# Optimization experiments

Measured on AMD Instinct MI355X. Metric: run time of the kernel, lower is better.

Reference implementation:

```python
import jax, jax.numpy as jnp
import numpy as np

B, I, C, L, KS = 16, 64, 128, 16384, 5
CA_K = 5
K_CR = 76      # crucial channels: floor(0.6*128)=76, already even
EPS = 1e-5


def conv1d(x, w, pad):
    # x: [N, Cin, L], w: [Cout, Cin, K]
    return jax.lax.conv_general_dilated(
        x, w, window_strides=(1,), padding=[(pad, pad)],
        dimension_numbers=('NCH', 'OIH', 'NCH'))


def bn(x, g, b, m, v):
    # eval-mode BatchNorm1d over channel dim of [N, C, L]
    inv = g / jnp.sqrt(v + EPS)
    return x * inv[None, :, None] + (b - m * inv)[None, :, None]


def setup_inputs() -> dict:
    key = jax.random.key(0)
    ks = jax.random.split(key, 10)
    return {
        'x': jax.random.normal(ks[0], (B, I, L), jnp.float32),
        'conv_w': jax.random.normal(ks[1], (C, I, KS), jnp.float32) / np.sqrt(I * KS).astype(np.float32),
        'conv_b': jax.random.normal(ks[2], (C,), jnp.float32) * 0.01,
        'bn_g': jnp.ones((C,), jnp.float32) + jax.random.normal(ks[3], (C,), jnp.float32) * 0.05,
        'bn_b': jax.random.normal(ks[4], (C,), jnp.float32) * 0.05,
        'bn_m': jax.random.normal(ks[5], (C,), jnp.float32) * 0.05,
        'bn_v': jnp.ones((C,), jnp.float32) + jax.random.uniform(ks[6], (C,), jnp.float32) * 0.1,
        'alpha': jnp.float32(0.5),
        'beta': jnp.float32(0.5),
        'ca_w': jax.random.normal(ks[7], (1, 1, CA_K), jnp.float32) / np.sqrt(CA_K).astype(np.float32),
        'ca_b': jnp.zeros((1,), jnp.float32),
        'sa_w': jax.random.normal(ks[8], (1, 2, 7), jnp.float32) / np.sqrt(14.0).astype(np.float32),
        'sabn_g': jnp.ones((1,), jnp.float32) + jax.random.normal(ks[9], (1,), jnp.float32) * 0.05,
        'sabn_b': jnp.zeros((1,), jnp.float32),
        'sabn_m': jnp.zeros((1,), jnp.float32),
        'sabn_v': jnp.ones((1,), jnp.float32),
    }


def reference(x, conv_w, conv_b, bn_g, bn_b, bn_m, bn_v, alpha, beta,
              ca_w, ca_b, sa_w, sabn_g, sabn_b, sabn_m, sabn_v):
    # ---- conv_layer: Conv1d + BN + ReLU ----
    f = conv1d(x, conv_w, KS // 2) + conv_b[None, :, None]      # [B,C,L]
    f = jax.nn.relu(bn(f, bn_g, bn_b, bn_m, bn_v))

    # ---- ChannelAttention ----
    F_avg = jnp.mean(f, axis=2, keepdims=True)                  # [B,C,1]
    F_max = jnp.max(f, axis=2, keepdims=True)                   # [B,C,1]
    F_add = alpha * F_avg + 0.5 * (F_avg + F_max) + beta * F_max
    z = conv1d(F_add.transpose(0, 2, 1), ca_w, CA_K // 2) + ca_b[None, :, None]  # [B,1,C]
    channel_map = jax.nn.sigmoid(z.transpose(0, 2, 1))          # [B,C,1]

    crf = f * channel_map                                       # channel refined features

    # ---- SpatialAttention: topk channel split + scatter masks ----
    cm = channel_map[:, :, 0]                                   # [B,C]
    _, idx = jax.lax.top_k(cm, K_CR)                            # [B,K_CR]
    cru = jnp.zeros_like(cm).at[jnp.arange(B)[:, None], idx].set(1.0)[:, :, None]  # [B,C,1]
    sub = 1.0 - cru

    cf = cru * crf                                              # crucial features [B,C,L]
    sf = sub * crf                                              # subcrucial features

    c_max = jnp.max(cf, axis=1, keepdims=True)                  # [B,1,L]
    c_avg = jnp.mean(cf, axis=1, keepdims=True) * (C / K_CR)
    s_max = jnp.max(sf, axis=1, keepdims=True)
    s_avg = jnp.mean(sf, axis=1, keepdims=True) * (C / (C - K_CR))

    def gate(mx, av):
        y = conv1d(jnp.concatenate([mx, av], axis=1), sa_w, 3)  # [B,1,L]
        return jax.nn.sigmoid(jax.nn.relu(bn(y, sabn_g, sabn_b, sabn_m, sabn_v)))

    A1 = gate(c_max, c_avg)
    A2 = gate(s_max, s_avg)
    return cf * A1 + sf * A2                                    # [B,C,L]
```

## Files before the change

kernel.cpp:

```cpp
#include <hip/hip_runtime.h>
#include <hip/hip_bf16.h>
#include <math.h>

#define BB 16
#define IC 64
#define CH 128
#define LL 16384
#define KS 5
#define CAK 5
#define KCR 76
#define EPSV 1e-5f
#define NLT2 256

typedef short bf16x8 __attribute__((ext_vector_type(8)));
typedef float f32x16 __attribute__((ext_vector_type(16)));

#define OFF_WPACK 0
#define OFF_BIAS2 40960
#define OFF_PSUM  (OFF_BIAS2 + CH)
#define OFF_PMAX  (OFF_PSUM + BB*CH*NLT2)
#define OFF_CM    (OFF_PMAX + BB*CH*NLT2)
#define OFF_MASK  (OFF_CM + BB*CH)
#define OFF_A1    (OFF_MASK + BB*CH)
#define OFF_A2    (OFF_A1 + BB*LL)
#define OFF_F16   (OFF_A2 + BB*LL)
#define WS_NEED_FLOATS ((size_t)OFF_F16 + (size_t)BB * CH * LL / 2)

__device__ __forceinline__ unsigned short f2bf(float f) {
    union { float f; unsigned u; } v; v.f = f;
    return (unsigned short)((v.u + 0x7FFFu + ((v.u >> 16) & 1u)) >> 16);
}
__device__ __forceinline__ float bf2f(unsigned short h) {
    union { unsigned u; float f; } v; v.u = ((unsigned)h) << 16;
    return v.f;
}
__device__ __forceinline__ unsigned short f2h(float f) {
    _Float16 h = (_Float16)f;
    return __builtin_bit_cast(unsigned short, h);
}
__device__ __forceinline__ float h2f(unsigned short u) {
    _Float16 h = __builtin_bit_cast(_Float16, u);
    return (float)h;
}

template<int CTRL>
__device__ __forceinline__ float dppf(float v) {
    return __builtin_bit_cast(float,
        __builtin_amdgcn_update_dpp(0, __builtin_bit_cast(int, v), CTRL, 0xF, 0xF, true));
}
__device__ __forceinline__ float dpp_sum32(float s) {
    s += dppf<0x111>(s);
    s += dppf<0x112>(s);
    s += dppf<0x114>(s);
    s += dppf<0x118>(s);
    s += dppf<0x142>(s);
    return s;
}
__device__ __forceinline__ float dpp_max32(float m) {
    m = fmaxf(m, dppf<0x111>(m));
    m = fmaxf(m, dppf<0x112>(m));
    m = fmaxf(m, dppf<0x114>(m));
    m = fmaxf(m, dppf<0x118>(m));
    m = fmaxf(m, dppf<0x142>(m));
    return m;
}

__global__ void prep_kernel(const float* __restrict__ conv_w, const float* __restrict__ conv_b,
                            const float* __restrict__ bn_g, const float* __restrict__ bn_b,
                            const float* __restrict__ bn_m, const float* __restrict__ bn_v,
                            unsigned short* __restrict__ wpack, float* __restrict__ bias2)
{
    int e = blockIdx.x * 256 + threadIdx.x;
    if (e < 8 * 20 * 64 * 8) {
        int j    = e & 7;
        int ln   = (e >> 3) & 63;
        int rest = e >> 9;
        int s    = rest % 20;
        int mt   = (rest / 20) & 1;
        int ch2  = (rest / 40) & 1;
        int ver  = rest / 80;
        int c  = ch2 * 64 + mt * 32 + (ln & 31);
        int kk = s >> 2;
        int i  = (s & 3) * 16 + (ln >> 5) * 8 + j;
        float inv = bn_g[c] * rsqrtf(bn_v[c] + EPSV);
        float w = conv_w[(c * IC + i) * KS + kk] * inv;
        unsigned short h = f2bf(w);
        wpack[e] = (ver == 0) ? h : f2bf(w - bf2f(h));
    }
    if (e < CH) {
        float inv = bn_g[e] * rsqrtf(bn_v[e] + EPSV);
        bias2[e] = (conv_b[e] - bn_m[e]) * inv + bn_b[e];
    }
}

template<bool F16OUT>
__global__ __launch_bounds__(256, 4)
void conv_mfma_kernel(const float* __restrict__ x,
                      const unsigned short* __restrict__ wpack,
                      const float* __restrict__ bias2,
                      void* __restrict__ fout,
                      float* __restrict__ psum, float* __restrict__ pmax)
{
    __shared__ unsigned short xs[136 * 128];
    const int b   = blockIdx.x;
    const int lt  = blockIdx.y;
    const int l0  = lt * 128;
    const int tid = threadIdx.x;
    const int ln  = tid & 63;
    const int wv  = __builtin_amdgcn_readfirstlane(tid >> 6);

    const float* xb = x + (size_t)b * (IC * LL);
    const int ibase = wv * 16;
    #pragma unroll
    for (int g = 0; g < 3; ++g) {
        int row = g * 64 + ln;
        int l   = l0 - 4 + row;
        if (row < 136) {
            bool vl = (l >= 0) && (l < LL);
            float v[16];
            #pragma unroll
            for (int q = 0; q < 16; ++q)
                v[q] = vl ? xb[(size_t)(ibase + q) * LL + l] : 0.0f;
            int rs = row & 7;
            #pragma unroll
            for (int q2 = 0; q2 < 4; ++q2) {
                unsigned short h[4], lo[4];
                #pragma unroll
                for (int j = 0; j < 4; ++j) {
                    float vv = v[q2 * 4 + j];
                    h[j]  = f2bf(vv);
                    lo[j] = f2bf(vv - bf2f(h[j]));
                }
                int i0   = ibase + q2 * 4;
                int cc   = (i0 >> 3) ^ rs;
                int epos = row * 128 + cc * 8 + (i0 & 7);
                uint2 wh, wl;
                wh.x = (unsigned)h[0]  | ((unsigned)h[1]  << 16);
                wh.y = (unsigned)h[2]  | ((unsigned)h[3]  << 16);
                wl.x = (unsigned)lo[0] | ((unsigned)lo[1] << 16);
                wl.y = (unsigned)lo[2] | ((unsigned)lo[3] << 16);
                *(uint2*)&xs[epos]      = wh;
                *(uint2*)&xs[epos + 64] = wl;
            }
        }
    }
    __syncthreads();

    const int ch2  = wv >> 1;
    const int lh   = wv & 1;
    const int ln31 = ln & 31;
    const int hi   = ln >> 5;
    const int rowbase = lh * 64 + ln31 + 2;

    const unsigned short* wp  = wpack + (size_t)ln * 8;
    const unsigned short* pA0 = wp + (size_t)((ch2 * 2 + 0) * 20) * 512;
    const unsigned short* pA1 = wp + (size_t)((ch2 * 2 + 1) * 20) * 512;
    const unsigned short* pA2 = wp + (size_t)(((2 + ch2) * 2 + 0) * 20) * 512;
    const unsigned short* pA3 = wp + (size_t)(((2 + ch2) * 2 + 1) * 20) * 512;

    f32x16 acc[2][2];
    #pragma unroll
    for (int mt = 0; mt < 2; ++mt)
        #pragma unroll
        for (int nt = 0; nt < 2; ++nt)
            #pragma unroll
            for (int r = 0; r < 16; ++r) acc[mt][nt][r] = 0.0f;

    auto loadA = [&](bf16x8* Av, int s) {
        Av[0] = *(const bf16x8*)(pA0 + (size_t)s * 512);
        Av[1] = *(const bf16x8*)(pA1 + (size_t)s * 512);
        Av[2] = *(const bf16x8*)(pA2 + (size_t)s * 512);
        Av[3] = *(const bf16x8*)(pA3 + (size_t)s * 512);
    };
    auto loadB = [&](bf16x8* Bv, int s) {
        int kk = s >> 2, iq = s & 3;
        int r0 = rowbase + kk;
        int r1 = r0 + 32;
        int c0 = ((iq << 1) + hi) ^ (r0 & 7);
        int c1 = ((iq << 1) + hi) ^ (r1 & 7);
        Bv[0] = *(const bf16x8*)&xs[r0 * 128 + c0 * 8];
        Bv[1] = *(const bf16x8*)&xs[r0 * 128 + 64 + c0 * 8];
        Bv[2] = *(const bf16x8*)&xs[r1 * 128 + c1 * 8];
        Bv[3] = *(const bf16x8*)&xs[r1 * 128 + 64 + c1 * 8];
    };
    auto compute = [&](const bf16x8* Av, const bf16x8* Bv) {
        acc[0][0] = __builtin_amdgcn_mfma_f32_32x32x16_bf16(Av[0], Bv[0], acc[0][0], 0, 0, 0);
        acc[1][0] = __builtin_amdgcn_mfma_f32_32x32x16_bf16(Av[1], Bv[0], acc[1][0], 0, 0, 0);
        acc[0][1] = __builtin_amdgcn_mfma_f32_32x32x16_bf16(Av[0], Bv[2], acc[0][1], 0, 0, 0);
        acc[1][1] = __builtin_amdgcn_mfma_f32_32x32x16_bf16(Av[1], Bv[2], acc[1][1], 0, 0, 0);
        acc[0][0] = __builtin_amdgcn_mfma_f32_32x32x16_bf16(Av[0], Bv[1], acc[0][0], 0, 0, 0);
        acc[1][0] = __builtin_amdgcn_mfma_f32_32x32x16_bf16(Av[1], Bv[1], acc[1][0], 0, 0, 0);
        acc[0][1] = __builtin_amdgcn_mfma_f32_32x32x16_bf16(Av[0], Bv[3], acc[0][1], 0, 0, 0);
        acc[1][1] = __builtin_amdgcn_mfma_f32_32x32x16_bf16(Av[1], Bv[3], acc[1][1], 0, 0, 0);
        acc[0][0] = __builtin_amdgcn_mfma_f32_32x32x16_bf16(Av[2], Bv[0], acc[0][0], 0, 0, 0);
        acc[1][0] = __builtin_amdgcn_mfma_f32_32x32x16_bf16(Av[3], Bv[0], acc[1][0], 0, 0, 0);
        acc[0][1] = __builtin_amdgcn_mfma_f32_32x32x16_bf16(Av[2], Bv[2], acc[0][1], 0, 0, 0);
        acc[1][1] = __builtin_amdgcn_mfma_f32_32x32x16_bf16(Av[3], Bv[2], acc[1][1], 0, 0, 0);
    };

    bf16x8 Ar[3][4], Br[2][4];
    loadA(Ar[0], 0); loadA(Ar[1], 1); loadA(Ar[2], 2);
    loadB(Br[0], 0); loadB(Br[1], 1);
    #pragma unroll
    for (int s = 0; s < 20; ++s) {
        compute(Ar[s % 3], Br[s & 1]);
        if (s + 3 < 20) loadA(Ar[s % 3], s + 3);
        if (s + 2 < 20) loadB(Br[s & 1], s + 2);
    }

    const int lgbase = l0 + lh * 64 + ln31;
    #pragma unroll
    for (int mt = 0; mt < 2; ++mt) {
        #pragma unroll
        for (int nt = 0; nt < 2; ++nt) {
            #pragma unroll
            for (int r = 0; r < 16; ++r) {
                int c = ch2 * 64 + mt * 32 + (r & 3) + 8 * (r >> 2) + 4 * hi;
                float fv = fmaxf(acc[mt][nt][r] + bias2[c], 0.0f);
                size_t off = ((size_t)(b * CH + c)) * LL + lgbase + nt * 32;
                if constexpr (F16OUT) ((unsigned short*)fout)[off] = f2h(fv);
                else                  ((float*)fout)[off] = fv;
                acc[mt][nt][r] = fv;
            }
        }
    }
    #pragma unroll
    for (int mt = 0; mt < 2; ++mt) {
        #pragma unroll
        for (int r = 0; r < 16; ++r) {
            float s = dpp_sum32(acc[mt][0][r] + acc[mt][1][r]);
            float m = dpp_max32(fmaxf(acc[mt][0][r], acc[mt][1][r]));
            if (ln31 == 31) {
                int c   = ch2 * 64 + mt * 32 + (r & 3) + 8 * (r >> 2) + 4 * hi;
                int lt2 = lt * 2 + lh;
                psum[(b * CH + c) * NLT2 + lt2] = s;
                pmax[(b * CH + c) * NLT2 + lt2] = m;
            }
        }
    }
}

__global__ void chan_kernel(const float* __restrict__ psum, const float* __restrict__ pmax,
                            const float* __restrict__ alpha, const float* __restrict__ beta,
                            const float* __restrict__ ca_w, const float* __restrict__ ca_b,
                            float* __restrict__ cm, float* __restrict__ maskv)
{
    int b = blockIdx.x;
    int c = threadIdx.x;
    const float* ps = psum + (b * CH + c) * NLT2;
    const float* pm = pmax + (b * CH + c) * NLT2;
    float s = 0.0f, m = 0.0f;
    for (int t = 0; t < NLT2; ++t) { s += ps[t]; m = fmaxf(m, pm[t]); }
    float favg = s * (1.0f / LL);
    float fadd = (alpha[0] + 0.5f) * favg + (beta[0] + 0.5f) * m;

    __shared__ float fa[CH];
    __shared__ float cms[CH];
    fa[c] = fadd;
    __syncthreads();

    float z = ca_b[0];
    #pragma unroll
    for (int k = 0; k < CAK; ++k) {
        int cc = c + k - 2;
        float v = (cc >= 0 && cc < CH) ? fa[cc] : 0.0f;
        z = fmaf(ca_w[k], v, z);
    }
    float cmv = 1.0f / (1.0f + expf(-z));
    cms[c] = cmv;
    __syncthreads();

    int rank = 0;
    for (int cc = 0; cc < CH; ++cc) {
        float o = cms[cc];
        rank += (o > cmv || (o == cmv && cc < c)) ? 1 : 0;
    }
    cm[b * CH + c] = cmv;
    maskv[b * CH + c] = (rank < KCR) ? 1.0f : 0.0f;
}

__global__ __launch_bounds__(256)
void sgf_kernel(const unsigned short* __restrict__ f16, float* __restrict__ out,
                const float* __restrict__ cm, const float* __restrict__ maskv,
                const float* __restrict__ sa_w,
                const float* __restrict__ sabn_g, const float* __restrict__ sabn_b,
                const float* __restrict__ sabn_m, const float* __restrict__ sabn_v)
{
    __shared__ float cms[CH], mks[CH];
    __shared__ float st[4][520];
    const int g   = blockIdx.x;
    const int b   = blockIdx.y;
    const int l0  = g * 512;
    const int tid = threadIdx.x;
    if (tid < CH) { cms[tid] = cm[b * CH + tid]; mks[tid] = maskv[b * CH + tid]; }
    __syncthreads();

    {
        const unsigned short* fb = f16 + (size_t)b * CH * LL + l0 + 2 * tid;
        float cmx0 = 0.f, csm0 = 0.f, smx0 = 0.f, ssm0 = 0.f;
        float cmx1 = 0.f, csm1 = 0.f, smx1 = 0.f, ssm1 = 0.f;
        #pragma unroll 4
        for (int c = 0; c < CH; ++c) {
            unsigned pr = *(const unsigned*)(fb + (size_t)c * LL);
            float cmc = cms[c], mk = mks[c];
            float v0 = h2f((unsigned short)(pr & 0xFFFFu)) * cmc;
            float v1 = h2f((unsigned short)(pr >> 16)) * cmc;
            float vs0 = v0 * mk, vu0 = v0 - vs0;
            float vs1 = v1 * mk, vu1 = v1 - vs1;
            cmx0 = fmaxf(cmx0, vs0); smx0 = fmaxf(smx0, vu0); csm0 += vs0; ssm0 += vu0;
            cmx1 = fmaxf(cmx1, vs1); smx1 = fmaxf(smx1, vu1); csm1 += vs1; ssm1 += vu1;
        }
        int s0 = 3 + 2 * tid;
        st[0][s0] = cmx0;                  st[0][s0 + 1] = cmx1;
        st[1][s0] = csm0 * (1.0f / KCR);   st[1][s0 + 1] = csm1 * (1.0f / KCR);
        st[2][s0] = smx0;                  st[2][s0 + 1] = smx1;
        st[3][s0] = ssm0 * (1.0f / (CH - KCR));
        st[3][s0 + 1] = ssm1 * (1.0f / (CH - KCR));
    }
    if (tid < 6) {
        int slot = (tid < 3) ? tid : 515 + (tid - 3);
        int l = l0 - 3 + slot;
        float cmx = 0.f, csm = 0.f, smx = 0.f, ssm = 0.f;
        if (l >= 0 && l < LL) {
            const unsigned short* fb = f16 + (size_t)b * CH * LL + l;
            for (int c = 0; c < CH; ++c) {
                float v  = h2f(fb[(size_t)c * LL]) * cms[c];
                float mk = mks[c];
                float vs = v * mk, vu = v - vs;
                cmx = fmaxf(cmx, vs); smx = fmaxf(smx, vu);
                csm += vs; ssm += vu;
            }
        }
        st[0][slot] = cmx;
        st[1][slot] = csm * (1.0f / KCR);
        st[2][slot] = smx;
        st[3][slot] = ssm * (1.0f / (CH - KCR));
    }
    __syncthreads();

    float inv = sabn_g[0] * rsqrtf(sabn_v[0] + EPSV);
    float bb2 = sabn_b[0] - sabn_m[0] * inv;
    float y1a = 0.f, y2a = 0.f, y1b = 0.f, y2b = 0.f;
    #pragma unroll
    for (int k = 0; k < 7; ++k) {
        float wm = sa_w[k], wa = sa_w[7 + k];
        int s0 = 2 * tid + k;
        y1a = fmaf(wm, st[0][s0],     fmaf(wa, st[1][s0],     y1a));
        y2a = fmaf(wm, st[2][s0],     fmaf(wa, st[3][s0],     y2a));
        y1b = fmaf(wm, st[0][s0 + 1], fmaf(wa, st[1][s0 + 1], y1b));
        y2b = fmaf(wm, st[2][s0 + 1], fmaf(wa, st[3][s0 + 1], y2b));
    }
    float A1a = 1.0f / (1.0f + expf(-fmaxf(y1a * inv + bb2, 0.f)));
    float A2a = 1.0f / (1.0f + expf(-fmaxf(y2a * inv + bb2, 0.f)));
    float A1b = 1.0f / (1.0f + expf(-fmaxf(y1b * inv + bb2, 0.f)));
    float A2b = 1.0f / (1.0f + expf(-fmaxf(y2b * inv + bb2, 0.f)));

    const unsigned short* fb = f16 + (size_t)b * CH * LL + l0 + 2 * tid;
    float* ob = out + (size_t)b * CH * LL + l0 + 2 * tid;
    #pragma unroll 4
    for (int c = 0; c < CH; ++c) {
        unsigned pr = *(const unsigned*)(fb + (size_t)c * LL);
        float cmc = cms[c];
        float v0 = h2f((unsigned short)(pr & 0xFFFFu)) * cmc;
        float v1 = h2f((unsigned short)(pr >> 16)) * cmc;
        bool sel = (mks[c] > 0.5f);
        float2 w;
        w.x = v0 * (sel ? A1a : A2a);
        w.y = v1 * (sel ? A1b : A2b);
        *(float2*)(ob + (size_t)c * LL) = w;
    }
}

__global__ __launch_bounds__(256)
void stats_gate_kernel(const float* __restrict__ f, const float* __restrict__ cm,
                       const float* __restrict__ maskv, const float* __restrict__ sa_w,
                       const float* __restrict__ sabn_g, const float* __restrict__ sabn_b,
                       const float* __restrict__ sabn_m, const float* __restrict__ sabn_v,
                       float* __restrict__ A1, float* __restrict__ A2)
{
    __shared__ float cms[CH], mks[CH];
    __shared__ float st[4][264];
    int b   = blockIdx.x;
    int l0  = blockIdx.y * 256;
    int tid = threadIdx.x;
    if (tid < CH) { cms[tid] = cm[b * CH + tid]; mks[tid] = maskv[b * CH + tid]; }
    __syncthreads();

    for (int idx = tid; idx < 262; idx += 256) {
        int l = l0 - 3 + idx;
        float cmx = 0.f, csm = 0.f, smx = 0.f, ssm = 0.f;
        if (l >= 0 && l < LL) {
            const float* fb = f + (size_t)b * CH * LL + l;
            #pragma unroll 4
            for (int c = 0; c < CH; ++c) {
                float v  = fb[(size_t)c * LL] * cms[c];
                float mk = mks[c];
                float vs = v * mk;
                float vu = v - vs;
                cmx = fmaxf(cmx, vs);
                smx = fmaxf(smx, vu);
                csm += vs;
                ssm += vu;
            }
        }
        st[0][idx] = cmx;
        st[1][idx] = csm * (1.0f / KCR);
        st[2][idx] = smx;
        st[3][idx] = ssm * (1.0f / (CH - KCR));
    }
    __syncthreads();

    float inv = sabn_g[0] * rsqrtf(sabn_v[0] + EPSV);
    float bb2 = sabn_b[0] - sabn_m[0] * inv;
    float y1 = 0.f, y2 = 0.f;
    #pragma unroll
    for (int k = 0; k < 7; ++k) {
        float wm = sa_w[k], wa = sa_w[7 + k];
        y1 = fmaf(wm, st[0][tid + k], fmaf(wa, st[1][tid + k], y1));
        y2 = fmaf(wm, st[2][tid + k], fmaf(wa, st[3][tid + k], y2));
    }
    float t1 = fmaxf(y1 * inv + bb2, 0.f);
    float t2 = fmaxf(y2 * inv + bb2, 0.f);
    A1[b * LL + l0 + tid] = 1.0f / (1.0f + expf(-t1));
    A2[b * LL + l0 + tid] = 1.0f / (1.0f + expf(-t2));
}

__global__ __launch_bounds__(256)
void final_kernel(float* __restrict__ out, const float* __restrict__ cm,
                  const float* __restrict__ maskv,
                  const float* __restrict__ A1, const float* __restrict__ A2)
{
    int g = blockIdx.x * 256 + threadIdx.x;
    size_t idx4 = (size_t)g * 4;
    int l  = (int)(idx4 & (LL - 1));
    int bc = (int)(idx4 >> 14);
    int b  = bc >> 7;
    float cmv = cm[bc];
    float mk  = maskv[bc];
    const float* Ap = (mk > 0.5f) ? A1 : A2;
    float4 a = *(const float4*)&Ap[b * LL + l];
    float4 v = *(const float4*)&out[idx4];
    v.x *= cmv * a.x;
    v.y *= cmv * a.y;
    v.z *= cmv * a.z;
    v.w *= cmv * a.w;
    *(float4*)&out[idx4] = v;
}

extern "C" void kernel_launch(void* const* d_in, const int* in_sizes, int n_in,
                              void* d_out, int out_size, void* d_ws, size_t ws_size,
                              hipStream_t stream)
{
    const float* x      = (const float*)d_in[0];
    const float* conv_w = (const float*)d_in[1];
    const float* conv_b = (const float*)d_in[2];
    const float* bn_g   = (const float*)d_in[3];
    const float* bn_b   = (const float*)d_in[4];
    const float* bn_m   = (const float*)d_in[5];
    const float* bn_v   = (const float*)d_in[6];
    const float* alpha  = (const float*)d_in[7];
    const float* beta   = (const float*)d_in[8];
    const float* ca_w   = (const float*)d_in[9];
    const float* ca_b   = (const float*)d_in[10];
    const float* sa_w   = (const float*)d_in[11];
    const float* sabn_g = (const float*)d_in[12];
    const float* sabn_b = (const float*)d_in[13];
    const float* sabn_m = (const float*)d_in[14];
    const float* sabn_v = (const float*)d_in[15];

    float* out = (float*)d_out;
    float* ws  = (float*)d_ws;

    unsigned short* wpack = (unsigned short*)(ws + OFF_WPACK);
    float* bias2 = ws + OFF_BIAS2;
    float* psum  = ws + OFF_PSUM;
    float* pmax  = ws + OFF_PMAX;
    float* cmv_  = ws + OFF_CM;
    float* mskv  = ws + OFF_MASK;
    float* A1p   = ws + OFF_A1;
    float* A2p   = ws + OFF_A2;
    unsigned short* f16p = (unsigned short*)(ws + OFF_F16);

    const bool fp16_path = (ws_size >= WS_NEED_FLOATS * sizeof(float));

    prep_kernel<<<320, 256, 0, stream>>>(conv_w, conv_b, bn_g, bn_b, bn_m, bn_v, wpack, bias2);

    if (fp16_path) {
        conv_mfma_kernel<true><<<dim3(BB, 128), 256, 0, stream>>>(x, wpack, bias2,
                                                                  (void*)f16p, psum, pmax);
        chan_kernel<<<BB, CH, 0, stream>>>(psum, pmax, alpha, beta, ca_w, ca_b, cmv_, mskv);
        sgf_kernel<<<dim3(32, BB), 256, 0, stream>>>(f16p, out, cmv_, mskv, sa_w,
                                                     sabn_g, sabn_b, sabn_m, sabn_v);
    } else {
        conv_mfma_kernel<false><<<dim3(BB, 128), 256, 0, stream>>>(x, wpack, bias2,
                                                                   (void*)out, psum, pmax);
        chan_kernel<<<BB, CH, 0, stream>>>(psum, pmax, alpha, beta, ca_w, ca_b, cmv_, mskv);
        stats_gate_kernel<<<dim3(BB, 64), 256, 0, stream>>>(out, cmv_, mskv, sa_w,
                                                            sabn_g, sabn_b, sabn_m, sabn_v, A1p, A2p);
        final_kernel<<<(BB * CH * LL / 4 + 255) / 256, 256, 0, stream>>>(out, cmv_, mskv, A1p, A2p);
    }
}
```

Before: 167.7 us.

## Use single fp16 MFMA conv and recompute channel max in fp32 for candidates

```diff
diff --git a/kernel.cpp b/kernel.cpp
--- a/kernel.cpp
+++ b/kernel.cpp
@@ -11,29 +11,21 @@
 #define KCR 76
 #define EPSV 1e-5f
 #define NLT2 256
-
-typedef short bf16x8 __attribute__((ext_vector_type(8)));
+#define EPSR 8e-3f
+
+typedef _Float16 f16x8 __attribute__((ext_vector_type(8)));
 typedef float f32x16 __attribute__((ext_vector_type(16)));
 
 #define OFF_WPACK 0
-#define OFF_BIAS2 40960
+#define OFF_W2F   20480
+#define OFF_BIAS2 (OFF_W2F + 40960)
 #define OFF_PSUM  (OFF_BIAS2 + CH)
 #define OFF_PMAX  (OFF_PSUM + BB*CH*NLT2)
-#define OFF_CM    (OFF_PMAX + BB*CH*NLT2)
+#define OFF_FADD  (OFF_PMAX + BB*CH*NLT2)
+#define OFF_CM    (OFF_FADD + BB*CH)
 #define OFF_MASK  (OFF_CM + BB*CH)
-#define OFF_A1    (OFF_MASK + BB*CH)
-#define OFF_A2    (OFF_A1 + BB*LL)
-#define OFF_F16   (OFF_A2 + BB*LL)
-#define WS_NEED_FLOATS ((size_t)OFF_F16 + (size_t)BB * CH * LL / 2)
-
-__device__ __forceinline__ unsigned short f2bf(float f) {
-    union { float f; unsigned u; } v; v.f = f;
-    return (unsigned short)((v.u + 0x7FFFu + ((v.u >> 16) & 1u)) >> 16);
-}
-__device__ __forceinline__ float bf2f(unsigned short h) {
-    union { unsigned u; float f; } v; v.u = ((unsigned)h) << 16;
-    return v.f;
-}
+#define OFF_F16   (OFF_MASK + BB*CH)
+
 __device__ __forceinline__ unsigned short f2h(float f) {
     _Float16 h = (_Float16)f;
     return __builtin_bit_cast(unsigned short, h);
@@ -68,24 +60,29 @@
 __global__ void prep_kernel(const float* __restrict__ conv_w, const float* __restrict__ conv_b,
                             const float* __restrict__ bn_g, const float* __restrict__ bn_b,
                             const float* __restrict__ bn_m, const float* __restrict__ bn_v,
-                            unsigned short* __restrict__ wpack, float* __restrict__ bias2)
+                            unsigned short* __restrict__ wpack, float* __restrict__ w2f,
+                            float* __restrict__ bias2)
 {
     int e = blockIdx.x * 256 + threadIdx.x;
-    if (e < 8 * 20 * 64 * 8) {
+    if (e < 4 * 20 * 64 * 8) {
         int j    = e & 7;
         int ln   = (e >> 3) & 63;
         int rest = e >> 9;
         int s    = rest % 20;
         int mt   = (rest / 20) & 1;
-        int ch2  = (rest / 40) & 1;
-        int ver  = rest / 80;
+        int ch2  = rest / 40;
         int c  = ch2 * 64 + mt * 32 + (ln & 31);
         int kk = s >> 2;
         int i  = (s & 3) * 16 + (ln >> 5) * 8 + j;
         float inv = bn_g[c] * rsqrtf(bn_v[c] + EPSV);
-        float w = conv_w[(c * IC + i) * KS + kk] * inv;
-        unsigned short h = f2bf(w);
-        wpack[e] = (ver == 0) ? h : f2bf(w - bf2f(h));
+        wpack[e] = f2h(conv_w[(c * IC + i) * KS + kk] * inv);
+    }
+    if (e < CH * KS * IC) {
+        int i  = e & 63;
+        int kk = (e >> 6) % KS;
+        int c  = e / (KS * IC);
+        float inv = bn_g[c] * rsqrtf(bn_v[c] + EPSV);
+        w2f[e] = conv_w[(c * IC + i) * KS + kk] * inv;
     }
     if (e < CH) {
         float inv = bn_g[e] * rsqrtf(bn_v[e] + EPSV);
@@ -93,15 +90,14 @@
     }
 }
 
-template<bool F16OUT>
 __global__ __launch_bounds__(256, 4)
 void conv_mfma_kernel(const float* __restrict__ x,
                       const unsigned short* __restrict__ wpack,
                       const float* __restrict__ bias2,
-                      void* __restrict__ fout,
+                      unsigned short* __restrict__ f16,
                       float* __restrict__ psum, float* __restrict__ pmax)
 {
-    __shared__ unsigned short xs[136 * 128];
+    __shared__ unsigned short xs[136 * 64];
     const int b   = blockIdx.x;
     const int lt  = blockIdx.y;
     const int l0  = lt * 128;
@@ -121,26 +117,20 @@
             #pragma unroll
             for (int q = 0; q < 16; ++q)
                 v[q] = vl ? xb[(size_t)(ibase + q) * LL + l] : 0.0f;
+            unsigned short h[16];
+            #pragma unroll
+            for (int q = 0; q < 16; ++q) h[q] = f2h(v[q]);
             int rs = row & 7;
             #pragma unroll
-            for (int q2 = 0; q2 < 4; ++q2) {
-                unsigned short h[4], lo[4];
-                #pragma unroll
-                for (int j = 0; j < 4; ++j) {
-                    float vv = v[q2 * 4 + j];
-                    h[j]  = f2bf(vv);
-                    lo[j] = f2bf(vv - bf2f(h[j]));
-                }
-                int i0   = ibase + q2 * 4;
-                int cc   = (i0 >> 3) ^ rs;
-                int epos = row * 128 + cc * 8 + (i0 & 7);
-                uint2 wh, wl;
-                wh.x = (unsigned)h[0]  | ((unsigned)h[1]  << 16);
-                wh.y = (unsigned)h[2]  | ((unsigned)h[3]  << 16);
-                wl.x = (unsigned)lo[0] | ((unsigned)lo[1] << 16);
-                wl.y = (unsigned)lo[2] | ((unsigned)lo[3] << 16);
-                *(uint2*)&xs[epos]      = wh;
-                *(uint2*)&xs[epos + 64] = wl;
+            for (int q2 = 0; q2 < 2; ++q2) {
+                int i0    = ibase + q2 * 8;
+                int chunk = (i0 >> 3) ^ rs;
+                uint4 w4;
+                w4.x = (unsigned)h[q2*8+0] | ((unsigned)h[q2*8+1] << 16);
+                w4.y = (unsigned)h[q2*8+2] | ((unsigned)h[q2*8+3] << 16);
+                w4.z = (unsigned)h[q2*8+4] | ((unsigned)h[q2*8+5] << 16);
+                w4.w = (unsigned)h[q2*8+6] | ((unsigned)h[q2*8+7] << 16);
+                *(uint4*)&xs[row * 64 + chunk * 8] = w4;
             }
         }
     }
@@ -155,8 +145,6 @@
     const unsigned short* wp  = wpack + (size_t)ln * 8;
     const unsigned short* pA0 = wp + (size_t)((ch2 * 2 + 0) * 20) * 512;
     const unsigned short* pA1 = wp + (size_t)((ch2 * 2 + 1) * 20) * 512;
-    const unsigned short* pA2 = wp + (size_t)(((2 + ch2) * 2 + 0) * 20) * 512;
-    const unsigned short* pA3 = wp + (size_t)(((2 + ch2) * 2 + 1) * 20) * 512;
 
     f32x16 acc[2][2];
     #pragma unroll
@@ -166,46 +154,32 @@
             #pragma unroll
             for (int r = 0; r < 16; ++r) acc[mt][nt][r] = 0.0f;
 
-    auto loadA = [&](bf16x8* Av, int s) {
-        Av[0] = *(const bf16x8*)(pA0 + (size_t)s * 512);
-        Av[1] = *(const bf16x8*)(pA1 + (size_t)s * 512);
-        Av[2] = *(const bf16x8*)(pA2 + (size_t)s * 512);
-        Av[3] = *(const bf16x8*)(pA3 + (size_t)s * 512);
+    auto loadA = [&](f16x8* Av, int s) {
+        Av[0] = *(const f16x8*)(pA0 + (size_t)s * 512);
+        Av[1] = *(const f16x8*)(pA1 + (size_t)s * 512);
     };
-    auto loadB = [&](bf16x8* Bv, int s) {
+    auto loadB = [&](f16x8* Bv, int s) {
         int kk = s >> 2, iq = s & 3;
         int r0 = rowbase + kk;
         int r1 = r0 + 32;
         int c0 = ((iq << 1) + hi) ^ (r0 & 7);
         int c1 = ((iq << 1) + hi) ^ (r1 & 7);
-        Bv[0] = *(const bf16x8*)&xs[r0 * 128 + c0 * 8];
-        Bv[1] = *(const bf16x8*)&xs[r0 * 128 + 64 + c0 * 8];
-        Bv[2] = *(const bf16x8*)&xs[r1 * 128 + c1 * 8];
-        Bv[3] = *(const bf16x8*)&xs[r1 * 128 + 64 + c1 * 8];
+        Bv[0] = *(const f16x8*)&xs[r0 * 64 + c0 * 8];
+        Bv[1] = *(const f16x8*)&xs[r1 * 64 + c1 * 8];
     };
-    auto compute = [&](const bf16x8* Av, const bf16x8* Bv) {
-        acc[0][0] = __builtin_amdgcn_mfma_f32_32x32x16_bf16(Av[0], Bv[0], acc[0][0], 0, 0, 0);
-        acc[1][0] = __builtin_amdgcn_mfma_f32_32x32x16_bf16(Av[1], Bv[0], acc[1][0], 0, 0, 0);
-        acc[0][1] = __builtin_amdgcn_mfma_f32_32x32x16_bf16(Av[0], Bv[2], acc[0][1], 0, 0, 0);
-        acc[1][1] = __builtin_amdgcn_mfma_f32_32x32x16_bf16(Av[1], Bv[2], acc[1][1], 0, 0, 0);
-        acc[0][0] = __builtin_amdgcn_mfma_f32_32x32x16_bf16(Av[0], Bv[1], acc[0][0], 0, 0, 0);
-        acc[1][0] = __builtin_amdgcn_mfma_f32_32x32x16_bf16(Av[1], Bv[1], acc[1][0], 0, 0, 0);
-        acc[0][1] = __builtin_amdgcn_mfma_f32_32x32x16_bf16(Av[0], Bv[3], acc[0][1], 0, 0, 0);
-        acc[1][1] = __builtin_amdgcn_mfma_f32_32x32x16_bf16(Av[1], Bv[3], acc[1][1], 0, 0, 0);
-        acc[0][0] = __builtin_amdgcn_mfma_f32_32x32x16_bf16(Av[2], Bv[0], acc[0][0], 0, 0, 0);
-        acc[1][0] = __builtin_amdgcn_mfma_f32_32x32x16_bf16(Av[3], Bv[0], acc[1][0], 0, 0, 0);
-        acc[0][1] = __builtin_amdgcn_mfma_f32_32x32x16_bf16(Av[2], Bv[2], acc[0][1], 0, 0, 0);
-        acc[1][1] = __builtin_amdgcn_mfma_f32_32x32x16_bf16(Av[3], Bv[2], acc[1][1], 0, 0, 0);
+    auto compute = [&](const f16x8* Av, const f16x8* Bv) {
+        acc[0][0] = __builtin_amdgcn_mfma_f32_32x32x16_f16(Av[0], Bv[0], acc[0][0], 0, 0, 0);
+        acc[1][0] = __builtin_amdgcn_mfma_f32_32x32x16_f16(Av[1], Bv[0], acc[1][0], 0, 0, 0);
+        acc[0][1] = __builtin_amdgcn_mfma_f32_32x32x16_f16(Av[0], Bv[1], acc[0][1], 0, 0, 0);
+        acc[1][1] = __builtin_amdgcn_mfma_f32_32x32x16_f16(Av[1], Bv[1], acc[1][1], 0, 0, 0);
     };
 
-    bf16x8 Ar[3][4], Br[2][4];
-    loadA(Ar[0], 0); loadA(Ar[1], 1); loadA(Ar[2], 2);
-    loadB(Br[0], 0); loadB(Br[1], 1);
+    f16x8 Ar[2][2], Br[2][2];
+    loadA(Ar[0], 0); loadB(Br[0], 0);
     #pragma unroll
     for (int s = 0; s < 20; ++s) {
-        compute(Ar[s % 3], Br[s & 1]);
-        if (s + 3 < 20) loadA(Ar[s % 3], s + 3);
-        if (s + 2 < 20) loadB(Br[s & 1], s + 2);
+        if (s + 1 < 20) { loadA(Ar[(s + 1) & 1], s + 1); loadB(Br[(s + 1) & 1], s + 1); }
+        compute(Ar[s & 1], Br[s & 1]);
     }
 
     const int lgbase = l0 + lh * 64 + ln31;
@@ -217,9 +191,7 @@
             for (int r = 0; r < 16; ++r) {
                 int c = ch2 * 64 + mt * 32 + (r & 3) + 8 * (r >> 2) + 4 * hi;
                 float fv = fmaxf(acc[mt][nt][r] + bias2[c], 0.0f);
-                size_t off = ((size_t)(b * CH + c)) * LL + lgbase + nt * 32;
-                if constexpr (F16OUT) ((unsigned short*)fout)[off] = f2h(fv);
-                else                  ((float*)fout)[off] = fv;
+                f16[((size_t)(b * CH + c)) * LL + lgbase + nt * 32] = f2h(fv);
                 acc[mt][nt][r] = fv;
             }
         }
@@ -240,23 +212,82 @@
     }
 }
 
-__global__ void chan_kernel(const float* __restrict__ psum, const float* __restrict__ pmax,
-                            const float* __restrict__ alpha, const float* __restrict__ beta,
-                            const float* __restrict__ ca_w, const float* __restrict__ ca_b,
-                            float* __restrict__ cm, float* __restrict__ maskv)
+__global__ __launch_bounds__(64)
+void fixmax_kernel(const float* __restrict__ x, const float* __restrict__ w2f,
+                   const float* __restrict__ bias2,
+                   const float* __restrict__ psum, const float* __restrict__ pmax,
+                   const float* __restrict__ alpha, const float* __restrict__ beta,
+                   float* __restrict__ fadd)
+{
+    const int c  = blockIdx.x;
+    const int b  = blockIdx.y;
+    const int ln = threadIdx.x;
+    const float* ps = psum + (size_t)(b * CH + c) * NLT2;
+    const float* pm = pmax + (size_t)(b * CH + c) * NLT2;
+
+    float pmg[4], s4 = 0.0f, m4 = 0.0f;
+    #pragma unroll
+    for (int g = 0; g < 4; ++g) {
+        pmg[g] = pm[g * 64 + ln];
+        s4 += ps[g * 64 + ln];
+        m4 = fmaxf(m4, pmg[g]);
+    }
+    float stot = s4, M = m4;
+    #pragma unroll
+    for (int off = 1; off <= 32; off <<= 1) {
+        stot += __shfl_xor(stot, off, 64);
+        M = fmaxf(M, __shfl_xor(M, off, 64));
+    }
+
+    const float* xb  = x + (size_t)b * (IC * LL);
+    const float* w2c = w2f + (size_t)c * (KS * IC);
+    const float bsc  = bias2[c];
+    float Fmax = 0.0f;
+    int cnt = 0;
+    #pragma unroll
+    for (int g = 0; g < 4 && cnt < 8; ++g) {
+        unsigned long long bal = __ballot(pmg[g] >= M - EPSR);
+        while (bal && cnt < 8) {
+            int sl = __ffsll((long long)bal) - 1;
+            bal &= bal - 1;
+            ++cnt;
+            int slot = g * 64 + sl;
+            int l    = (slot >> 1) * 128 + (slot & 1) * 64 + ln;
+            float fe = bsc;
+            #pragma unroll
+            for (int kk = 0; kk < KS; ++kk) {
+                int lidx = l + kk - 2;
+                bool v = (lidx >= 0) && (lidx < LL);
+                const float* xr = xb + lidx;
+                const float* wr = w2c + kk * IC;
+                for (int i = 0; i < IC; ++i) {
+                    float xv = v ? xr[(size_t)i * LL] : 0.0f;
+                    fe = fmaf(xv, wr[i], fe);
+                }
+            }
+            fe = fmaxf(fe, 0.0f);
+            #pragma unroll
+            for (int off = 1; off <= 32; off <<= 1)
+                fe = fmaxf(fe, __shfl_xor(fe, off, 64));
+            Fmax = fmaxf(Fmax, fe);
+        }
+    }
+
+    if (ln == 0) {
+        float favg = stot * (1.0f / LL);
+        fadd[b * CH + c] = (alpha[0] + 0.5f) * favg + (beta[0] + 0.5f) * Fmax;
+    }
+}
+
+__global__ void chan2_kernel(const float* __restrict__ fadd,
+                             const float* __restrict__ ca_w, const float* __restrict__ ca_b,
+                             float* __restrict__ cm, float* __restrict__ maskv)
 {
     int b = blockIdx.x;
     int c = threadIdx.x;
-    const float* ps = psum + (b * CH + c) * NLT2;
-    const float* pm = pmax + (b * CH + c) * NLT2;
-    float s = 0.0f, m = 0.0f;
-    for (int t = 0; t < NLT2; ++t) { s += ps[t]; m = fmaxf(m, pm[t]); }
-    float favg = s * (1.0f / LL);
-    float fadd = (alpha[0] + 0.5f) * favg + (beta[0] + 0.5f) * m;
-
     __shared__ float fa[CH];
     __shared__ float cms[CH];
-    fa[c] = fadd;
+    fa[c] = fadd[b * CH + c];
     __syncthreads();
 
     float z = ca_b[0];
@@ -369,82 +400,6 @@
         w.y = v1 * (sel ? A1b : A2b);
         *(float2*)(ob + (size_t)c * LL) = w;
     }
-}
-
-__global__ __launch_bounds__(256)
-void stats_gate_kernel(const float* __restrict__ f, const float* __restrict__ cm,
-                       const float* __restrict__ maskv, const float* __restrict__ sa_w,
-                       const float* __restrict__ sabn_g, const float* __restrict__ sabn_b,
-                       const float* __restrict__ sabn_m, const float* __restrict__ sabn_v,
-                       float* __restrict__ A1, float* __restrict__ A2)
-{
-    __shared__ float cms[CH], mks[CH];
-    __shared__ float st[4][264];
-    int b   = blockIdx.x;
-    int l0  = blockIdx.y * 256;
-    int tid = threadIdx.x;
-    if (tid < CH) { cms[tid] = cm[b * CH + tid]; mks[tid] = maskv[b * CH + tid]; }
-    __syncthreads();
-
-    for (int idx = tid; idx < 262; idx += 256) {
-        int l = l0 - 3 + idx;
-        float cmx = 0.f, csm = 0.f, smx = 0.f, ssm = 0.f;
-        if (l >= 0 && l < LL) {
-            const float* fb = f + (size_t)b * CH * LL + l;
-            #pragma unroll 4
-            for (int c = 0; c < CH; ++c) {
-                float v  = fb[(size_t)c * LL] * cms[c];
-                float mk = mks[c];
-                float vs = v * mk;
-                float vu = v - vs;
-                cmx = fmaxf(cmx, vs);
-                smx = fmaxf(smx, vu);
-                csm += vs;
-                ssm += vu;
-            }
-        }
-        st[0][idx] = cmx;
-        st[1][idx] = csm * (1.0f / KCR);
-        st[2][idx] = smx;
-        st[3][idx] = ssm * (1.0f / (CH - KCR));
-    }
-    __syncthreads();
-
-    float inv = sabn_g[0] * rsqrtf(sabn_v[0] + EPSV);
-    float bb2 = sabn_b[0] - sabn_m[0] * inv;
-    float y1 = 0.f, y2 = 0.f;
-    #pragma unroll
-    for (int k = 0; k < 7; ++k) {
-        float wm = sa_w[k], wa = sa_w[7 + k];
-        y1 = fmaf(wm, st[0][tid + k], fmaf(wa, st[1][tid + k], y1));
-        y2 = fmaf(wm, st[2][tid + k], fmaf(wa, st[3][tid + k], y2));
-    }
-    float t1 = fmaxf(y1 * inv + bb2, 0.f);
-    float t2 = fmaxf(y2 * inv + bb2, 0.f);
-    A1[b * LL + l0 + tid] = 1.0f / (1.0f + expf(-t1));
-    A2[b * LL + l0 + tid] = 1.0f / (1.0f + expf(-t2));
-}
-
-__global__ __launch_bounds__(256)
-void final_kernel(float* __restrict__ out, const float* __restrict__ cm,
-                  const float* __restrict__ maskv,
-                  const float* __restrict__ A1, const float* __restrict__ A2)
-{
-    int g = blockIdx.x * 256 + threadIdx.x;
-    size_t idx4 = (size_t)g * 4;
-    int l  = (int)(idx4 & (LL - 1));
-    int bc = (int)(idx4 >> 14);
-    int b  = bc >> 7;
-    float cmv = cm[bc];
-    float mk  = maskv[bc];
-    const float* Ap = (mk > 0.5f) ? A1 : A2;
-    float4 a = *(const float4*)&Ap[b * LL + l];
-    float4 v = *(const float4*)&out[idx4];
-    v.x *= cmv * a.x;
-    v.y *= cmv * a.y;
-    v.z *= cmv * a.z;
-    v.w *= cmv * a.w;
-    *(float4*)&out[idx4] = v;
 }
 
 extern "C" void kernel_launch(void* const* d_in, const int* in_sizes, int n_in,
@@ -472,31 +427,25 @@
     float* ws  = (float*)d_ws;
 
     unsigned short* wpack = (unsigned short*)(ws + OFF_WPACK);
+    float* w2f   = ws + OFF_W2F;
     float* bias2 = ws + OFF_BIAS2;
     float* psum  = ws + OFF_PSUM;
     float* pmax  = ws + OFF_PMAX;
+    float* faddp = ws + OFF_FADD;
     float* cmv_  = ws + OFF_CM;
     float* mskv  = ws + OFF_MASK;
-    float* A1p   = ws + OFF_A1;
-    float* A2p   = ws + OFF_A2;
     unsigned short* f16p = (unsigned short*)(ws + OFF_F16);
 
-    const bool fp16_path = (ws_size >= WS_NEED_FLOATS * sizeof(float));
-
-    prep_kernel<<<320, 256, 0, stream>>>(conv_w, conv_b, bn_g, bn_b, bn_m, bn_v, wpack, bias2);
-
-    if (fp16_path) {
-        conv_mfma_kernel<true><<<dim3(BB, 128), 256, 0, stream>>>(x, wpack, bias2,
-                                                                  (void*)f16p, psum, pmax);
-        chan_kernel<<<BB, CH, 0, stream>>>(psum, pmax, alpha, beta, ca_w, ca_b, cmv_, mskv);
-        sgf_kernel<<<dim3(32, BB), 256, 0, stream>>>(f16p, out, cmv_, mskv, sa_w,
-                                                     sabn_g, sabn_b, sabn_m, sabn_v);
-    } else {
-        conv_mfma_kernel<false><<<dim3(BB, 128), 256, 0, stream>>>(x, wpack, bias2,
-                                                                   (void*)out, psum, pmax);
-        chan_kernel<<<BB, CH, 0, stream>>>(psum, pmax, alpha, beta, ca_w, ca_b, cmv_, mskv);
-        stats_gate_kernel<<<dim3(BB, 64), 256, 0, stream>>>(out, cmv_, mskv, sa_w,
-                                                            sabn_g, sabn_b, sabn_m, sabn_v, A1p, A2p);
-        final_kernel<<<(BB * CH * LL / 4 + 255) / 256, 256, 0, stream>>>(out, cmv_, mskv, A1p, A2p);
-    }
-}
+    prep_kernel<<<160, 256, 0, stream>>>(conv_w, conv_b, bn_g, bn_b, bn_m, bn_v,
+                                         wpack, w2f, bias2);
+
+    conv_mfma_kernel<<<dim3(BB, 128), 256, 0, stream>>>(x, wpack, bias2, f16p, psum, pmax);
+
+    fixmax_kernel<<<dim3(CH, BB), 64, 0, stream>>>(x, w2f, bias2, psum, pmax,
+                                                   alpha, beta, faddp);
+
+    chan2_kernel<<<BB, CH, 0, stream>>>(faddp, ca_w, ca_b, cmv_, mskv);
+
+    sgf_kernel<<<dim3(32, BB), 256, 0, stream>>>(f16p, out, cmv_, mskv, sa_w,
+                                                 sabn_g, sabn_b, sabn_m, sabn_v);
+}
```

New measurement: 193.2 us. +15.2%, slower.

## Pre-convert input to bf16 hi/lo layout and double-buffer conv tiles via global_load_lds

Applied to the files above, without the earlier changes.

```diff
diff --git a/kernel.cpp b/kernel.cpp
--- a/kernel.cpp
+++ b/kernel.cpp
@@ -11,6 +11,8 @@
 #define KCR 76
 #define EPSV 1e-5f
 #define NLT2 256
+#define GROWS 8
+#define XROWS (LL + 2 * GROWS)
 
 typedef short bf16x8 __attribute__((ext_vector_type(8)));
 typedef float f32x16 __attribute__((ext_vector_type(16)));
@@ -21,10 +23,7 @@
 #define OFF_PMAX  (OFF_PSUM + BB*CH*NLT2)
 #define OFF_CM    (OFF_PMAX + BB*CH*NLT2)
 #define OFF_MASK  (OFF_CM + BB*CH)
-#define OFF_A1    (OFF_MASK + BB*CH)
-#define OFF_A2    (OFF_A1 + BB*LL)
-#define OFF_F16   (OFF_A2 + BB*LL)
-#define WS_NEED_FLOATS ((size_t)OFF_F16 + (size_t)BB * CH * LL / 2)
+#define OFF_F16   (OFF_MASK + BB*CH)
 
 __device__ __forceinline__ unsigned short f2bf(float f) {
     union { float f; unsigned u; } v; v.f = f;
@@ -41,6 +40,13 @@
 __device__ __forceinline__ float h2f(unsigned short u) {
     _Float16 h = __builtin_bit_cast(_Float16, u);
     return (float)h;
+}
+
+__device__ __forceinline__ void gload16(const void* g, void* l) {
+    __builtin_amdgcn_global_load_lds(
+        (const __attribute__((address_space(1))) void*)g,
+        (__attribute__((address_space(3))) void*)l,
+        16, 0, 0);
 }
 
 template<int CTRL>
@@ -93,58 +99,79 @@
     }
 }
 
-template<bool F16OUT>
-__global__ __launch_bounds__(256, 4)
-void conv_mfma_kernel(const float* __restrict__ x,
+__global__ void guard_kernel(unsigned short* __restrict__ xt)
+{
+    int b = blockIdx.x;
+    int t = threadIdx.x;
+    unsigned* p0 = (unsigned*)(xt + (size_t)b * XROWS * 128);
+    unsigned* p1 = (unsigned*)(xt + ((size_t)b * XROWS + GROWS + LL) * 128);
+    for (int k = t; k < GROWS * 64; k += 256) { p0[k] = 0; p1[k] = 0; }
+}
+
+__global__ __launch_bounds__(256)
+void prex_kernel(const float* __restrict__ x, unsigned short* __restrict__ xt)
+{
+    __shared__ float xtile[64][65];
+    const int lg  = blockIdx.x;
+    const int b   = blockIdx.y;
+    const int tid = threadIdx.x;
+    const int ln  = tid & 63;
+    const int wv4 = tid >> 6;
+
+    const float* xb = x + (size_t)b * IC * LL + (size_t)lg * 64;
+    #pragma unroll
+    for (int k = 0; k < 16; ++k) {
+        int i = wv4 * 16 + k;
+        xtile[i][ln] = xb[(size_t)i * LL + ln];
+    }
+    __syncthreads();
+
+    unsigned* xtb = (unsigned*)(xt + ((size_t)b * XROWS + GROWS + (size_t)lg * 64) * 128);
+    #pragma unroll
+    for (int k = 0; k < 16; ++k) {
+        int d  = tid + k * 256;
+        int r  = d >> 6;
+        int dd = d & 63;
+        int rs = ((lg * 64 + r) + 4) & 7;
+        int s0 = (dd & 31) * 2;
+        int ch = (s0 >> 3) ^ rs;
+        int i0 = (ch << 3) | (s0 & 7);
+        float v0 = xtile[i0][r];
+        float v1 = xtile[i0 + 1][r];
+        unsigned short h0 = f2bf(v0), h1 = f2bf(v1);
+        unsigned short u0, u1;
+        if (dd < 32) { u0 = h0; u1 = h1; }
+        else { u0 = f2bf(v0 - bf2f(h0)); u1 = f2bf(v1 - bf2f(h1)); }
+        xtb[(size_t)r * 64 + dd] = (unsigned)u0 | ((unsigned)u1 << 16);
+    }
+}
+
+__global__ __launch_bounds__(256, 2)
+void conv_mfma_kernel(const unsigned short* __restrict__ xt,
                       const unsigned short* __restrict__ wpack,
                       const float* __restrict__ bias2,
-                      void* __restrict__ fout,
+                      unsigned short* __restrict__ f16,
                       float* __restrict__ psum, float* __restrict__ pmax)
 {
-    __shared__ unsigned short xs[136 * 128];
+    __shared__ unsigned short xs[2][136 * 128];
     const int b   = blockIdx.x;
-    const int lt  = blockIdx.y;
-    const int l0  = lt * 128;
+    const int ltg = blockIdx.y;
     const int tid = threadIdx.x;
     const int ln  = tid & 63;
     const int wv  = __builtin_amdgcn_readfirstlane(tid >> 6);
 
-    const float* xb = x + (size_t)b * (IC * LL);
-    const int ibase = wv * 16;
-    #pragma unroll
-    for (int g = 0; g < 3; ++g) {
-        int row = g * 64 + ln;
-        int l   = l0 - 4 + row;
-        if (row < 136) {
-            bool vl = (l >= 0) && (l < LL);
-            float v[16];
-            #pragma unroll
-            for (int q = 0; q < 16; ++q)
-                v[q] = vl ? xb[(size_t)(ibase + q) * LL + l] : 0.0f;
-            int rs = row & 7;
-            #pragma unroll
-            for (int q2 = 0; q2 < 4; ++q2) {
-                unsigned short h[4], lo[4];
-                #pragma unroll
-                for (int j = 0; j < 4; ++j) {
-                    float vv = v[q2 * 4 + j];
-                    h[j]  = f2bf(vv);
-                    lo[j] = f2bf(vv - bf2f(h[j]));
-                }
-                int i0   = ibase + q2 * 4;
-                int cc   = (i0 >> 3) ^ rs;
-                int epos = row * 128 + cc * 8 + (i0 & 7);
-                uint2 wh, wl;
-                wh.x = (unsigned)h[0]  | ((unsigned)h[1]  << 16);
-                wh.y = (unsigned)h[2]  | ((unsigned)h[3]  << 16);
-                wl.x = (unsigned)lo[0] | ((unsigned)lo[1] << 16);
-                wl.y = (unsigned)lo[2] | ((unsigned)lo[3] << 16);
-                *(uint2*)&xs[epos]      = wh;
-                *(uint2*)&xs[epos + 64] = wl;
-            }
-        }
-    }
-    __syncthreads();
+    const unsigned short* xtb = xt + (size_t)b * XROWS * 128;
+
+    auto stage = [&](int buf, int tile) {
+        const char* src = (const char*)(xtb + ((size_t)tile * 128 + 4) * 128);
+        char* dst = (char*)&xs[buf][0];
+        #pragma unroll
+        for (int g0 = 0; g0 < 9; ++g0) {
+            int g = wv + g0 * 4;
+            if (g < 34)
+                gload16(src + (size_t)g * 1024 + (size_t)ln * 16, dst + g * 1024);
+        }
+    };
 
     const int ch2  = wv >> 1;
     const int lh   = wv & 1;
@@ -157,14 +184,6 @@
     const unsigned short* pA1 = wp + (size_t)((ch2 * 2 + 1) * 20) * 512;
     const unsigned short* pA2 = wp + (size_t)(((2 + ch2) * 2 + 0) * 20) * 512;
     const unsigned short* pA3 = wp + (size_t)(((2 + ch2) * 2 + 1) * 20) * 512;
-
-    f32x16 acc[2][2];
-    #pragma unroll
-    for (int mt = 0; mt < 2; ++mt)
-        #pragma unroll
-        for (int nt = 0; nt < 2; ++nt)
-            #pragma unroll
-            for (int r = 0; r < 16; ++r) acc[mt][nt][r] = 0.0f;
 
     auto loadA = [&](bf16x8* Av, int s) {
         Av[0] = *(const bf16x8*)(pA0 + (size_t)s * 512);
@@ -172,17 +191,19 @@
         Av[2] = *(const bf16x8*)(pA2 + (size_t)s * 512);
         Av[3] = *(const bf16x8*)(pA3 + (size_t)s * 512);
     };
-    auto loadB = [&](bf16x8* Bv, int s) {
+    auto loadB = [&](bf16x8* Bv, const unsigned short* bufp, int s) {
         int kk = s >> 2, iq = s & 3;
         int r0 = rowbase + kk;
         int r1 = r0 + 32;
         int c0 = ((iq << 1) + hi) ^ (r0 & 7);
         int c1 = ((iq << 1) + hi) ^ (r1 & 7);
-        Bv[0] = *(const bf16x8*)&xs[r0 * 128 + c0 * 8];
-        Bv[1] = *(const bf16x8*)&xs[r0 * 128 + 64 + c0 * 8];
-        Bv[2] = *(const bf16x8*)&xs[r1 * 128 + c1 * 8];
-        Bv[3] = *(const bf16x8*)&xs[r1 * 128 + 64 + c1 * 8];
+        Bv[0] = *(const bf16x8*)&bufp[r0 * 128 + c0 * 8];
+        Bv[1] = *(const bf16x8*)&bufp[r0 * 128 + 64 + c0 * 8];
+        Bv[2] = *(const bf16x8*)&bufp[r1 * 128 + c1 * 8];
+        Bv[3] = *(const bf16x8*)&bufp[r1 * 128 + 64 + c1 * 8];
     };
+
+    f32x16 acc[2][2];
     auto compute = [&](const bf16x8* Av, const bf16x8* Bv) {
         acc[0][0] = __builtin_amdgcn_mfma_f32_32x32x16_bf16(Av[0], Bv[0], acc[0][0], 0, 0, 0);
         acc[1][0] = __builtin_amdgcn_mfma_f32_32x32x16_bf16(Av[1], Bv[0], acc[1][0], 0, 0, 0);
@@ -198,45 +219,61 @@
         acc[1][1] = __builtin_amdgcn_mfma_f32_32x32x16_bf16(Av[3], Bv[2], acc[1][1], 0, 0, 0);
     };
 
-    bf16x8 Ar[3][4], Br[2][4];
-    loadA(Ar[0], 0); loadA(Ar[1], 1); loadA(Ar[2], 2);
-    loadB(Br[0], 0); loadB(Br[1], 1);
-    #pragma unroll
-    for (int s = 0; s < 20; ++s) {
-        compute(Ar[s % 3], Br[s & 1]);
-        if (s + 3 < 20) loadA(Ar[s % 3], s + 3);
-        if (s + 2 < 20) loadB(Br[s & 1], s + 2);
-    }
-
-    const int lgbase = l0 + lh * 64 + ln31;
-    #pragma unroll
-    for (int mt = 0; mt < 2; ++mt) {
+    stage(0, ltg * 4);
+    __syncthreads();
+
+    for (int t = 0; t < 4; ++t) {
+        if (t < 3) stage((t + 1) & 1, ltg * 4 + t + 1);
+
+        const unsigned short* bufp = &xs[t & 1][0];
         #pragma unroll
-        for (int nt = 0; nt < 2; ++nt) {
+        for (int mt = 0; mt < 2; ++mt)
+            #pragma unroll
+            for (int nt = 0; nt < 2; ++nt)
+                #pragma unroll
+                for (int r = 0; r < 16; ++r) acc[mt][nt][r] = 0.0f;
+
+        bf16x8 Ar[3][4], Br[2][4];
+        loadA(Ar[0], 0); loadA(Ar[1], 1); loadA(Ar[2], 2);
+        loadB(Br[0], bufp, 0); loadB(Br[1], bufp, 1);
+        #pragma unroll
+        for (int s = 0; s < 20; ++s) {
+            compute(Ar[s % 3], Br[s & 1]);
+            if (s + 3 < 20) loadA(Ar[s % 3], s + 3);
+            if (s + 2 < 20) loadB(Br[s & 1], bufp, s + 2);
+        }
+
+        const int ltile  = ltg * 4 + t;
+        const int lgbase = ltile * 128 + lh * 64 + ln31;
+        #pragma unroll
+        for (int mt = 0; mt < 2; ++mt) {
+            #pragma unroll
+            for (int nt = 0; nt < 2; ++nt) {
+                #pragma unroll
+                for (int r = 0; r < 16; ++r) {
+                    int c = ch2 * 64 + mt * 32 + (r & 3) + 8 * (r >> 2) + 4 * hi;
+                    float fv = fmaxf(acc[mt][nt][r] + bias2[c], 0.0f);
+                    f16[((size_t)(b * CH + c)) * LL + lgbase + nt * 32] = f2h(fv);
+                    acc[mt][nt][r] = fv;
+                }
+            }
+        }
+        #pragma unroll
+        for (int mt = 0; mt < 2; ++mt) {
             #pragma unroll
             for (int r = 0; r < 16; ++r) {
-                int c = ch2 * 64 + mt * 32 + (r & 3) + 8 * (r >> 2) + 4 * hi;
-                float fv = fmaxf(acc[mt][nt][r] + bias2[c], 0.0f);
-                size_t off = ((size_t)(b * CH + c)) * LL + lgbase + nt * 32;
-                if constexpr (F16OUT) ((unsigned short*)fout)[off] = f2h(fv);
-                else                  ((float*)fout)[off] = fv;
-                acc[mt][nt][r] = fv;
+                float s = dpp_sum32(acc[mt][0][r] + acc[mt][1][r]);
+                float m = dpp_max32(fmaxf(acc[mt][0][r], acc[mt][1][r]));
+                if (ln31 == 31) {
+                    int c   = ch2 * 64 + mt * 32 + (r & 3) + 8 * (r >> 2) + 4 * hi;
+                    int lt2 = ltile * 2 + lh;
+                    psum[(b * CH + c) * NLT2 + lt2] = s;
+                    pmax[(b * CH + c) * NLT2 + lt2] = m;
+                }
             }
         }
-    }
-    #pragma unroll
-    for (int mt = 0; mt < 2; ++mt) {
-        #pragma unroll
-        for (int r = 0; r < 16; ++r) {
-            float s = dpp_sum32(acc[mt][0][r] + acc[mt][1][r]);
-            float m = dpp_max32(fmaxf(acc[mt][0][r], acc[mt][1][r]));
-            if (ln31 == 31) {
-                int c   = ch2 * 64 + mt * 32 + (r & 3) + 8 * (r >> 2) + 4 * hi;
-                int lt2 = lt * 2 + lh;
-                psum[(b * CH + c) * NLT2 + lt2] = s;
-                pmax[(b * CH + c) * NLT2 + lt2] = m;
-            }
-        }
+
+        __syncthreads();
     }
 }
 
@@ -369,82 +406,6 @@
         w.y = v1 * (sel ? A1b : A2b);
         *(float2*)(ob + (size_t)c * LL) = w;
     }
-}
-
-__global__ __launch_bounds__(256)
-void stats_gate_kernel(const float* __restrict__ f, const float* __restrict__ cm,
-                       const float* __restrict__ maskv, const float* __restrict__ sa_w,
-                       const float* __restrict__ sabn_g, const float* __restrict__ sabn_b,
-                       const float* __restrict__ sabn_m, const float* __restrict__ sabn_v,
-                       float* __restrict__ A1, float* __restrict__ A2)
-{
-    __shared__ float cms[CH], mks[CH];
-    __shared__ float st[4][264];
-    int b   = blockIdx.x;
-    int l0  = blockIdx.y * 256;
-    int tid = threadIdx.x;
-    if (tid < CH) { cms[tid] = cm[b * CH + tid]; mks[tid] = maskv[b * CH + tid]; }
-    __syncthreads();
-
-    for (int idx = tid; idx < 262; idx += 256) {
-        int l = l0 - 3 + idx;
-        float cmx = 0.f, csm = 0.f, smx = 0.f, ssm = 0.f;
-        if (l >= 0 && l < LL) {
-            const float* fb = f + (size_t)b * CH * LL + l;
-            #pragma unroll 4
-            for (int c = 0; c < CH; ++c) {
-                float v  = fb[(size_t)c * LL] * cms[c];
-                float mk = mks[c];
-                float vs = v * mk;
-                float vu = v - vs;
-                cmx = fmaxf(cmx, vs);
-                smx = fmaxf(smx, vu);
-                csm += vs;
-                ssm += vu;
-            }
-        }
-        st[0][idx] = cmx;
-        st[1][idx] = csm * (1.0f / KCR);
-        st[2][idx] = smx;
-        st[3][idx] = ssm * (1.0f / (CH - KCR));
-    }
-    __syncthreads();
-
-    float inv = sabn_g[0] * rsqrtf(sabn_v[0] + EPSV);
-    float bb2 = sabn_b[0] - sabn_m[0] * inv;
-    float y1 = 0.f, y2 = 0.f;
-    #pragma unroll
-    for (int k = 0; k < 7; ++k) {
-        float wm = sa_w[k], wa = sa_w[7 + k];
-        y1 = fmaf(wm, st[0][tid + k], fmaf(wa, st[1][tid + k], y1));
-        y2 = fmaf(wm, st[2][tid + k], fmaf(wa, st[3][tid + k], y2));
-    }
-    float t1 = fmaxf(y1 * inv + bb2, 0.f);
-    float t2 = fmaxf(y2 * inv + bb2, 0.f);
-    A1[b * LL + l0 + tid] = 1.0f / (1.0f + expf(-t1));
-    A2[b * LL + l0 + tid] = 1.0f / (1.0f + expf(-t2));
-}
-
-__global__ __launch_bounds__(256)
-void final_kernel(float* __restrict__ out, const float* __restrict__ cm,
-                  const float* __restrict__ maskv,
-                  const float* __restrict__ A1, const float* __restrict__ A2)
-{
-    int g = blockIdx.x * 256 + threadIdx.x;
-    size_t idx4 = (size_t)g * 4;
-    int l  = (int)(idx4 & (LL - 1));
-    int bc = (int)(idx4 >> 14);
-    int b  = bc >> 7;
-    float cmv = cm[bc];
-    float mk  = maskv[bc];
-    const float* Ap = (mk > 0.5f) ? A1 : A2;
-    float4 a = *(const float4*)&Ap[b * LL + l];
-    float4 v = *(const float4*)&out[idx4];
-    v.x *= cmv * a.x;
-    v.y *= cmv * a.y;
-    v.z *= cmv * a.z;
-    v.w *= cmv * a.w;
-    *(float4*)&out[idx4] = v;
 }
 
 extern "C" void kernel_launch(void* const* d_in, const int* in_sizes, int n_in,
@@ -477,26 +438,21 @@
     float* pmax  = ws + OFF_PMAX;
     float* cmv_  = ws + OFF_CM;
     float* mskv  = ws + OFF_MASK;
-    float* A1p   = ws + OFF_A1;
-    float* A2p   = ws + OFF_A2;
     unsigned short* f16p = (unsigned short*)(ws + OFF_F16);
 
-    const bool fp16_path = (ws_size >= WS_NEED_FLOATS * sizeof(float));
-
-    prep_kernel<<<320, 256, 0, stream>>>(conv_w, conv_b, bn_g, bn_b, bn_m, bn_v, wpack, bias2);
-
-    if (fp16_path) {
-        conv_mfma_kernel<true><<<dim3(BB, 128), 256, 0, stream>>>(x, wpack, bias2,
-                                                                  (void*)f16p, psum, pmax);
-        chan_kernel<<<BB, CH, 0, stream>>>(psum, pmax, alpha, beta, ca_w, ca_b, cmv_, mskv);
-        sgf_kernel<<<dim3(32, BB), 256, 0, stream>>>(f16p, out, cmv_, mskv, sa_w,
-                                                     sabn_g, sabn_b, sabn_m, sabn_v);
-    } else {
-        conv_mfma_kernel<false><<<dim3(BB, 128), 256, 0, stream>>>(x, wpack, bias2,
-                                                                   (void*)out, psum, pmax);
-        chan_kernel<<<BB, CH, 0, stream>>>(psum, pmax, alpha, beta, ca_w, ca_b, cmv_, mskv);
-        stats_gate_kernel<<<dim3(BB, 64), 256, 0, stream>>>(out, cmv_, mskv, sa_w,
-                                                            sabn_g, sabn_b, sabn_m, sabn_v, A1p, A2p);
-        final_kernel<<<(BB * CH * LL / 4 + 255) / 256, 256, 0, stream>>>(out, cmv_, mskv, A1p, A2p);
-    }
-}
+    unsigned short* xt = (unsigned short*)d_out;
+
+    prep_kernel<<<320, 256, 0, stream>>>(conv_w, conv_b, bn_g, bn_b, bn_m, bn_v,
+                                         wpack, bias2);
+
+    guard_kernel<<<BB, 256, 0, stream>>>(xt);
+
+    prex_kernel<<<dim3(256, BB), 256, 0, stream>>>(x, xt);
+
+    conv_mfma_kernel<<<dim3(BB, 32), 256, 0, stream>>>(xt, wpack, bias2, f16p, psum, pmax);
+
+    chan_kernel<<<BB, CH, 0, stream>>>(psum, pmax, alpha, beta, ca_w, ca_b, cmv_, mskv);
+
+    sgf_kernel<<<dim3(32, BB), 256, 0, stream>>>(f16p, out, cmv_, mskv, sa_w,
+                                                 sabn_g, sabn_b, sabn_m, sabn_v);
+}
```

New measurement: 324.1 us. 1.93x slower.
